# Kernel tuning notes

Measured on AMD Instinct MI355X. Metric: run time of the kernel, lower is better.

Reference implementation:

```python
import jax, jax.numpy as jnp
import numpy as np

M, K, L, OUT = 16, 64, 6, 128
IN_CH = 2 + 1 + 1 + 1 + 4 * L  # 29
HID_IN = 128 * 2 + 4           # 260


def setup_inputs() -> dict:
    key = jax.random.key(0)
    ks = jax.random.split(key, 5)
    N = 2_000_000
    P = jax.random.normal(ks[0], (N, 2), jnp.float32) * 2.0
    def lin(k, i, o):
        return jax.random.normal(k, (i, o), jnp.float32) / np.float32(np.sqrt(i))
    return {
        'P': P,
        'W1': lin(ks[1], IN_CH, 64), 'b1': jnp.zeros((64,), jnp.float32),
        'W2': lin(ks[2], 64, 128),   'b2': jnp.zeros((128,), jnp.float32),
        'W3': lin(ks[3], HID_IN, 128), 'b3': jnp.zeros((128,), jnp.float32),
        'W4': lin(ks[4], 128, OUT),  'b4': jnp.zeros((OUT,), jnp.float32),
    }


def _fps(P, m):
    # furthest point sampling, seeded at index 0 (standard convention)
    N = P.shape[0]
    def step(carry, _):
        min_d, last_idx = carry
        last = P[last_idx]
        d = jnp.sum((P - last) ** 2, axis=-1)          # [N]
        min_d = jnp.minimum(min_d, d)
        nxt = jnp.argmax(min_d)
        return (min_d, nxt), last_idx
    init = (jnp.full((N,), jnp.finfo(jnp.float32).max, jnp.float32), jnp.int32(0))
    (_, _), idxs = jax.lax.scan(step, init, None, length=m)
    return idxs  # [m] int


def _gelu(x):
    return jax.nn.gelu(x, approximate=False)  # torch nn.GELU default = erf


def reference(P, W1, b1, W2, b2, W3, b3, W4, b4):
    c_idx = jax.lax.stop_gradient(_fps(P, M))
    C = P[c_idx]                                       # [M,2]
    # brute-force kNN: expanded squared distance avoids [M,N,2] intermediate
    Ps = jax.lax.stop_gradient(P)
    Cs = jax.lax.stop_gradient(C)
    d2 = (jnp.sum(Ps ** 2, -1)[None, :]
          - 2.0 * Cs @ Ps.T
          + jnp.sum(Cs ** 2, -1)[:, None])             # [M,N]
    _, nidx = jax.lax.top_k(-d2, K)                    # [M,K]
    patch = P[nidx]                                    # [M,K,2]
    delta = patch - C[:, None, :]                      # [M,K,2]
    r = jnp.linalg.norm(delta, axis=-1, keepdims=True) # [M,K,1]
    theta = jnp.arctan2(delta[..., 1:2], delta[..., 0:1])
    freqs = (2.0 ** jnp.arange(L)).astype(jnp.float32) # [L]
    ang = delta[..., None, :] * freqs[:, None]         # [M,K,L,2]
    ff = jnp.concatenate([jnp.sin(ang), jnp.cos(ang)], -1).reshape(M, K, 4 * L)
    per_pt = jnp.concatenate([delta, r, jnp.sin(theta), jnp.cos(theta), ff], -1)  # [M,K,29]
    h = _gelu(per_pt @ W1 + b1)
    h = _gelu(h @ W2 + b2)                             # [M,K,128]
    h_max = h.max(axis=1)
    h_mean = h.mean(axis=1)
    rr = r[..., 0]                                     # [M,K]
    stats = jnp.stack([rr.mean(1), rr.max(1), rr.min(1), rr.std(1, ddof=1)], -1)  # [M,4]
    z = jnp.concatenate([h_max, h_mean, stats], -1)    # [M,260]
    F = _gelu(z @ W3 + b3) @ W4 + b4                   # [M,OUT]
    return F, C
```

## Files before the change

kernel.cpp:

```cpp
#include <hip/hip_runtime.h>
#include <math.h>

#define MCENT 16
#define KNN   64
#define NBINS 512
#define RBINS 256
#define CAP   7936
#define SKEYS 1024
#define FPSB  512
#define FPST  256
#define NPT   16
#define MLPT  1024

__device__ __forceinline__ float gelu_f(float x){
    return 0.5f * x * (1.0f + erff(x * 0.70710678118654752440f));
}

__device__ __forceinline__ void xcd_slice(int NP, int B, int bid, int tpb, int tid,
                                          int* q0, int* s1, int* step){
    int xcd = bid & 7, j = bid >> 3, Bx = B >> 3;
    long long np = NP;
    *q0   = (int)((np * xcd) >> 3) + j*tpb + tid;
    *s1   = (int)((np * (xcd+1)) >> 3);
    *step = Bx * tpb;
}

__global__ void init_kernel(unsigned int* __restrict__ ghist,
                            unsigned int* __restrict__ cnt,
                            unsigned long long* __restrict__ partials){
    const int T = gridDim.x * blockDim.x;
    int t = blockIdx.x * blockDim.x + threadIdx.x;
    for (int i = t; i < MCENT*NBINS; i += T) ghist[i] = 0u;
    for (int i = t; i < (MCENT-1)*FPSB; i += T) partials[i] = 0ULL;
    if (t < MCENT) cnt[t] = 0u;
}

__global__ __launch_bounds__(FPST, 2) void fps_coop(
    const float* __restrict__ P, int N,
    unsigned long long* __restrict__ partials,
    float* __restrict__ cxy,
    float* __restrict__ outC)
{
    const int T = FPSB * FPST;
    const int t = blockIdx.x * FPST + threadIdx.x;
    const int lane = threadIdx.x & 63;
    const int wid  = threadIdx.x >> 6;

    float px[NPT], py[NPT], md[NPT];
#pragma unroll
    for (int i = 0; i < NPT; ++i){
        int g = t + i * T;
        if (g < N){
            float2 p = ((const float2*)P)[g];
            px[i] = p.x; py[i] = p.y; md[i] = 3.402823466e+38f;
        } else { px[i] = 0.f; py[i] = 0.f; md[i] = -1.0f; }
    }

    __shared__ unsigned long long wred[FPST/64];
    int cur = 0;

    for (int k = 0; k < MCENT; ++k){
        if (blockIdx.x == 0 && threadIdx.x == 0){
            float cx = P[2*cur], cy = P[2*cur+1];
            cxy[2*k] = cx; cxy[2*k+1] = cy;
            outC[2*k] = cx; outC[2*k+1] = cy;
        }
        if (k == MCENT-1) break;

        const float cx = P[2*cur], cy = P[2*cur+1];
        unsigned long long bk = 0ULL;
#pragma unroll
        for (int i = 0; i < NPT; ++i){
            float dx = __fsub_rn(px[i], cx);
            float dy = __fsub_rn(py[i], cy);
            float d  = __fadd_rn(__fmul_rn(dx,dx), __fmul_rn(dy,dy));
            if (md[i] >= 0.0f){
                float nm = fminf(md[i], d);
                md[i] = nm;
                unsigned long long key =
                    ((unsigned long long)__float_as_uint(nm) << 32)
                    | (unsigned long long)(0xFFFFFFFFu - (unsigned)(t + i*T));
                if (key > bk) bk = key;
            }
        }
#pragma unroll
        for (int off = 32; off > 0; off >>= 1){
            unsigned long long o = __shfl_xor(bk, off, 64);
            if (o > bk) bk = o;
        }
        if (lane == 0) wred[wid] = bk;
        __syncthreads();
        if (threadIdx.x == 0){
            unsigned long long b = wred[0];
#pragma unroll
            for (int w = 1; w < FPST/64; ++w) if (wred[w] > b) b = wred[w];
            __hip_atomic_store(&partials[k*FPSB + blockIdx.x], b,
                               __ATOMIC_RELEASE, __HIP_MEMORY_SCOPE_AGENT);
        }
        __syncthreads();

        unsigned long long pb = 0ULL;
        for (int i = threadIdx.x; i < FPSB; i += FPST){
            const unsigned long long* slot = &partials[k*FPSB + i];
            unsigned long long v = __hip_atomic_load(slot, __ATOMIC_RELAXED,
                                                     __HIP_MEMORY_SCOPE_AGENT);
            while (v == 0ULL){
                __builtin_amdgcn_s_sleep(1);
                v = __hip_atomic_load(slot, __ATOMIC_RELAXED,
                                      __HIP_MEMORY_SCOPE_AGENT);
            }
            if (v > pb) pb = v;
        }
#pragma unroll
        for (int off = 32; off > 0; off >>= 1){
            unsigned long long o = __shfl_xor(pb, off, 64);
            if (o > pb) pb = o;
        }
        if (lane == 0) wred[wid] = pb;
        __syncthreads();
        unsigned long long fin = wred[0];
#pragma unroll
        for (int w = 1; w < FPST/64; ++w) if (wred[w] > fin) fin = wred[w];
        __syncthreads();
        cur = (int)(0xFFFFFFFFu - (unsigned)(fin & 0xFFFFFFFFu));
    }
}

__global__ __launch_bounds__(256) void hist_kernel(
    const float* __restrict__ P, int N,
    const float* __restrict__ cxy,
    unsigned int* __restrict__ ghist,
    unsigned int* __restrict__ rhist)
{
    __shared__ unsigned int h[MCENT*NBINS];
    __shared__ float scx[MCENT], scy[MCENT], scs2[MCENT];
    {
        int gi = blockIdx.x*blockDim.x + threadIdx.x;
        if (gi < MCENT*RBINS) rhist[gi] = 0u;
    }
    for (int i = threadIdx.x; i < MCENT*NBINS; i += blockDim.x) h[i] = 0u;
    if (threadIdx.x < MCENT){
        float a = cxy[2*threadIdx.x], b = cxy[2*threadIdx.x+1];
        scx[threadIdx.x] = a; scy[threadIdx.x] = b;
        scs2[threadIdx.x] = __fadd_rn(__fmul_rn(a,a), __fmul_rn(b,b));
    }
    __syncthreads();
    const int T    = gridDim.x * blockDim.x;
    const int NP16 = (N >> 1) >> 4;
    for (int q = blockIdx.x*blockDim.x + threadIdx.x; q < NP16; q += T){
        float4 p = ((const float4*)P)[(size_t)q << 4];
        float ps20 = __fadd_rn(__fmul_rn(p.x,p.x), __fmul_rn(p.y,p.y));
        float ps21 = __fadd_rn(__fmul_rn(p.z,p.z), __fmul_rn(p.w,p.w));
#pragma unroll
        for (int m = 0; m < MCENT; ++m){
            float dot0 = __fadd_rn(__fmul_rn(scx[m],p.x), __fmul_rn(scy[m],p.y));
            float d20  = __fadd_rn(__fsub_rn(ps20, __fmul_rn(2.0f,dot0)), scs2[m]);
            atomicAdd(&h[m*NBINS + (__float_as_uint(fmaxf(d20,0.0f)) >> 22)], 1u);
            float dot1 = __fadd_rn(__fmul_rn(scx[m],p.z), __fmul_rn(scy[m],p.w));
            float d21  = __fadd_rn(__fsub_rn(ps21, __fmul_rn(2.0f,dot1)), scs2[m]);
            atomicAdd(&h[m*NBINS + (__float_as_uint(fmaxf(d21,0.0f)) >> 22)], 1u);
        }
    }
    __syncthreads();
    for (int i = threadIdx.x; i < MCENT*NBINS; i += blockDim.x){
        unsigned v = h[i];
        if (v) atomicAdd(&ghist[i], v);
    }
}

__global__ void thr_kernel(const unsigned int* __restrict__ ghist,
                           float* __restrict__ sc2){
    int m = threadIdx.x;
    if (m < MCENT){
        unsigned cum = 0; int B = NBINS-1;
        for (int b = 0; b < NBINS; ++b){
            cum += ghist[m*NBINS + b];
            if (cum >= KNN){ B = b; break; }
        }
        sc2[m] = 255.0f / __uint_as_float((unsigned)(B+1) << 22);
    }
}

__global__ __launch_bounds__(256) void refine_kernel(
    const float* __restrict__ P, int N,
    const float* __restrict__ cxy,
    const float* __restrict__ sc2,
    unsigned int* __restrict__ rhist)
{
    __shared__ unsigned int h[MCENT*RBINS];
    __shared__ float scx[MCENT], scy[MCENT], scs2[MCENT], ssc[MCENT];
    for (int i = threadIdx.x; i < MCENT*RBINS; i += 256) h[i] = 0u;
    if (threadIdx.x < MCENT){
        float a = cxy[2*threadIdx.x], b = cxy[2*threadIdx.x+1];
        scx[threadIdx.x]=a; scy[threadIdx.x]=b;
        scs2[threadIdx.x]=__fadd_rn(__fmul_rn(a,a),__fmul_rn(b,b));
        ssc[threadIdx.x]=sc2[threadIdx.x];
    }
    __syncthreads();
    const int NP = N >> 1;
    int q0, s1, st;
    xcd_slice(NP, gridDim.x, blockIdx.x, 256, threadIdx.x, &q0, &s1, &st);
    for (int q = q0; q < s1; q += st){
        float4 p = ((const float4*)P)[q];
        float ps20 = __fadd_rn(__fmul_rn(p.x,p.x), __fmul_rn(p.y,p.y));
        float ps21 = __fadd_rn(__fmul_rn(p.z,p.z), __fmul_rn(p.w,p.w));
#pragma unroll
        for (int m = 0; m < MCENT; ++m){
            float dot0 = __fadd_rn(__fmul_rn(scx[m],p.x), __fmul_rn(scy[m],p.y));
            float d20  = __fadd_rn(__fsub_rn(ps20, __fmul_rn(2.0f,dot0)), scs2[m]);
            int b0 = (int)(fmaxf(d20, 0.0f) * ssc[m]);
            if (b0 < RBINS) atomicAdd(&h[m*RBINS + b0], 1u);
            float dot1 = __fadd_rn(__fmul_rn(scx[m],p.z), __fmul_rn(scy[m],p.w));
            float d21  = __fadd_rn(__fsub_rn(ps21, __fmul_rn(2.0f,dot1)), scs2[m]);
            int b1 = (int)(fmaxf(d21, 0.0f) * ssc[m]);
            if (b1 < RBINS) atomicAdd(&h[m*RBINS + b1], 1u);
        }
    }
    if ((N & 1) && blockIdx.x == 0 && threadIdx.x == 0){
        int g = N-1;
        float x = P[2*g], y = P[2*g+1];
        float ps2 = __fadd_rn(__fmul_rn(x,x), __fmul_rn(y,y));
        for (int m = 0; m < MCENT; ++m){
            float dot = __fadd_rn(__fmul_rn(scx[m],x), __fmul_rn(scy[m],y));
            float d2  = __fadd_rn(__fsub_rn(ps2, __fmul_rn(2.0f,dot)), scs2[m]);
            int b = (int)(fmaxf(d2, 0.0f) * ssc[m]);
            if (b < RBINS) atomicAdd(&h[m*RBINS + b], 1u);
        }
    }
    __syncthreads();
    for (int i = threadIdx.x; i < MCENT*RBINS; i += blockDim.x){
        unsigned v = h[i];
        if (v) atomicAdd(&rhist[i], v);
    }
}

__global__ void thr2_kernel(const unsigned int* __restrict__ rhist,
                            int* __restrict__ B2){
    int m = threadIdx.x;
    if (m < MCENT){
        unsigned cum = 0; int B = RBINS-1;
        for (int b = 0; b < RBINS; ++b){
            cum += rhist[m*RBINS + b];
            if (cum >= KNN){ B = b; break; }
        }
        B2[m] = B;
    }
}

__global__ __launch_bounds__(256) void collect_kernel(
    const float* __restrict__ P, int N,
    const float* __restrict__ cxy,
    const float* __restrict__ sc2,
    const int* __restrict__ B2,
    unsigned int* __restrict__ cnt,
    float* __restrict__ cd2,
    int* __restrict__ cidx)
{
    __shared__ float scx[MCENT], scy[MCENT], scs2[MCENT], ssc[MCENT];
    __shared__ int sB2[MCENT];
    if (threadIdx.x < MCENT){
        float a = cxy[2*threadIdx.x], b = cxy[2*threadIdx.x+1];
        scx[threadIdx.x]=a; scy[threadIdx.x]=b;
        scs2[threadIdx.x]=__fadd_rn(__fmul_rn(a,a),__fmul_rn(b,b));
        ssc[threadIdx.x]=sc2[threadIdx.x];
        sB2[threadIdx.x]=B2[threadIdx.x];
    }
    __syncthreads();
    const int NP = N >> 1;
    int q0, s1, st;
    xcd_slice(NP, gridDim.x, blockIdx.x, 256, threadIdx.x, &q0, &s1, &st);
    for (int q = q0; q < s1; q += st){
        float4 p = ((const float4*)P)[q];
        float ps20 = __fadd_rn(__fmul_rn(p.x,p.x), __fmul_rn(p.y,p.y));
        float ps21 = __fadd_rn(__fmul_rn(p.z,p.z), __fmul_rn(p.w,p.w));
        int g = 2*q;
#pragma unroll
        for (int m = 0; m < MCENT; ++m){
            float dot0 = __fadd_rn(__fmul_rn(scx[m],p.x), __fmul_rn(scy[m],p.y));
            float d20  = __fadd_rn(__fsub_rn(ps20, __fmul_rn(2.0f,dot0)), scs2[m]);
            if ((int)(fmaxf(d20,0.0f) * ssc[m]) <= sB2[m]){
                unsigned pos = atomicAdd(&cnt[m], 1u);
                if (pos < CAP){ cd2[m*CAP+pos]=d20; cidx[m*CAP+pos]=g; }
            }
            float dot1 = __fadd_rn(__fmul_rn(scx[m],p.z), __fmul_rn(scy[m],p.w));
            float d21  = __fadd_rn(__fsub_rn(ps21, __fmul_rn(2.0f,dot1)), scs2[m]);
            if ((int)(fmaxf(d21,0.0f) * ssc[m]) <= sB2[m]){
                unsigned pos = atomicAdd(&cnt[m], 1u);
                if (pos < CAP){ cd2[m*CAP+pos]=d21; cidx[m*CAP+pos]=g+1; }
            }
        }
    }
    if ((N & 1) && blockIdx.x == 0 && threadIdx.x == 0){
        int g = N-1;
        float x = P[2*g], y = P[2*g+1];
        float ps2 = __fadd_rn(__fmul_rn(x,x), __fmul_rn(y,y));
        for (int m = 0; m < MCENT; ++m){
            float dot = __fadd_rn(__fmul_rn(scx[m],x), __fmul_rn(scy[m],y));
            float d2  = __fadd_rn(__fsub_rn(ps2, __fmul_rn(2.0f,dot)), scs2[m]);
            if ((int)(fmaxf(d2,0.0f) * ssc[m]) <= sB2[m]){
                unsigned pos = atomicAdd(&cnt[m], 1u);
                if (pos < CAP){ cd2[m*CAP+pos]=d2; cidx[m*CAP+pos]=g; }
            }
        }
    }
}

__global__ __launch_bounds__(MLPT) void mlp_kernel(
    const float* __restrict__ P,
    const float* __restrict__ cxy,
    const unsigned int* __restrict__ cnt,
    const float* __restrict__ cd2,
    const int* __restrict__ cidx,
    const float* __restrict__ W1, const float* __restrict__ b1,
    const float* __restrict__ W2, const float* __restrict__ b2,
    const float* __restrict__ W3, const float* __restrict__ b3,
    const float* __restrict__ W4, const float* __restrict__ b4,
    float* __restrict__ outF)
{
    const int m = blockIdx.x;
    const int tid = threadIdx.x;
    __shared__ float feat[KNN][32];
    __shared__ float h1s[KNN][64];
    __shared__ float sW1[29*64];
    __shared__ float sW2[64*128];
    __shared__ float pmax[8][128], psum[8][128];
    __shared__ float z[260];
    __shared__ float part[8][128];
    __shared__ float zz[128];
    __shared__ unsigned long long kkeys[SKEYS];
    __shared__ int snbr[KNN];

    {
        const float4* s2 = (const float4*)W2;
        float4* d2 = (float4*)sW2;
        d2[tid]        = s2[tid];
        d2[tid + 1024] = s2[tid + 1024];
        if (tid < 464) ((float4*)sW1)[tid] = ((const float4*)W1)[tid];
    }

    unsigned c = cnt[m]; if (c > CAP) c = CAP;
    if (c <= SKEYS){
        if (tid < (int)c){
            unsigned u = __float_as_uint(cd2[m*CAP+tid]);
            u = (u & 0x80000000u) ? ~u : (u | 0x80000000u);
            kkeys[tid] = ((unsigned long long)u << 32)
                       | (unsigned long long)(unsigned)cidx[m*CAP+tid];
        }
        __syncthreads();
        if (tid < (int)c){
            unsigned long long ki = kkeys[tid];
            int rank = 0;
            for (int j = 0; j < (int)c; ++j) rank += (kkeys[j] < ki);
            if (rank < KNN) snbr[rank] = (int)(unsigned)(ki & 0xFFFFFFFFu);
        }
    } else {
        for (int i = tid; i < (int)c; i += MLPT){
            unsigned ui = __float_as_uint(cd2[m*CAP+i]);
            ui = (ui & 0x80000000u) ? ~ui : (ui | 0x80000000u);
            unsigned long long ki = ((unsigned long long)ui << 32)
                                  | (unsigned long long)(unsigned)cidx[m*CAP+i];
            int rank = 0;
            for (int j = 0; j < (int)c; ++j){
                unsigned uj = __float_as_uint(cd2[m*CAP+j]);
                uj = (uj & 0x80000000u) ? ~uj : (uj | 0x80000000u);
                unsigned long long kj = ((unsigned long long)uj << 32)
                                      | (unsigned long long)(unsigned)cidx[m*CAP+j];
                rank += (kj < ki);
            }
            if (rank < KNN) snbr[rank] = (int)(unsigned)(ki & 0xFFFFFFFFu);
        }
    }
    __syncthreads();

    const float cx = cxy[2*m], cy = cxy[2*m+1];
    if (tid < KNN){
        int g = snbr[tid];
        float dx = P[2*g]   - cx;
        float dy = P[2*g+1] - cy;
        float r  = sqrtf(dx*dx + dy*dy);
        float th = atan2f(dy, dx);
        feat[tid][0]=dx; feat[tid][1]=dy; feat[tid][2]=r;
        feat[tid][3]=sinf(th); feat[tid][4]=cosf(th);
        float fx = dx, fy = dy;
#pragma unroll
        for (int l = 0; l < 6; ++l){
            feat[tid][5+4*l+0]=sinf(fx);
            feat[tid][5+4*l+1]=sinf(fy);
            feat[tid][5+4*l+2]=cosf(fx);
            feat[tid][5+4*l+3]=cosf(fy);
            fx += fx; fy += fy;
        }
    }
    __syncthreads();

#pragma unroll
    for (int rep = 0; rep < 4; ++rep){
        int o = rep*MLPT + tid;
        int k = o >> 6, j = o & 63;
        float acc = b1[j];
#pragma unroll
        for (int cc = 0; cc < 29; ++cc) acc += feat[k][cc] * sW1[cc*64 + j];
        h1s[k][j] = gelu_f(acc);
    }
    __syncthreads();

    {
        int j = tid & 127, kh = tid >> 7;
        float lmax = -3.402823466e+38f, lsum = 0.f;
        for (int kk = 0; kk < 8; ++kk){
            int k = kh*8 + kk;
            float acc = b2[j];
#pragma unroll 8
            for (int i = 0; i < 64; ++i) acc += h1s[k][i] * sW2[i*128 + j];
            float v = gelu_f(acc);
            lmax = fmaxf(lmax, v);
            lsum += v;
        }
        pmax[kh][j] = lmax; psum[kh][j] = lsum;
    }
    __syncthreads();
    if (tid < 128){
        float mx = pmax[0][tid], sm = psum[0][tid];
#pragma unroll
        for (int w = 1; w < 8; ++w){ mx = fmaxf(mx, pmax[w][tid]); sm += psum[w][tid]; }
        z[tid]       = mx;
        z[128 + tid] = sm * (1.0f/64.0f);
    }
    if (tid >= 128 && tid < 192){
        int l = tid - 128;
        float r = feat[l][2];
        float s = r, mx = r, mn = r;
        for (int off = 1; off < 64; off <<= 1){
            s  += __shfl_xor(s, off, 64);
            mx  = fmaxf(mx, __shfl_xor(mx, off, 64));
            mn  = fminf(mn, __shfl_xor(mn, off, 64));
        }
        float mean = s * (1.0f/64.0f);
        float dv = (r-mean)*(r-mean);
        for (int off = 1; off < 64; off <<= 1) dv += __shfl_xor(dv, off, 64);
        if (l == 0){
            z[256]=mean; z[257]=mx; z[258]=mn; z[259]=sqrtf(dv*(1.0f/63.0f));
        }
    }
    __syncthreads();

    {
        int j = tid & 127, seg = tid >> 7;
        int i0  = (seg < 4) ? seg*33 : 132 + (seg-4)*32;
        int cntn = (seg < 4) ? 33 : 32;
        float acc = 0.f;
        for (int i = i0; i < i0 + cntn; ++i) acc += z[i]*W3[i*128+j];
        part[seg][j] = acc;
    }
    __syncthreads();
    if (tid < 128){
        float a = part[0][tid];
#pragma unroll
        for (int w = 1; w < 8; ++w) a += part[w][tid];
        zz[tid] = gelu_f(a + b3[tid]);
    }
    __syncthreads();
    {
        int j = tid & 127, seg = tid >> 7;
        float acc = 0.f;
#pragma unroll
        for (int i = seg*16; i < seg*16+16; ++i) acc += zz[i]*W4[i*128+j];
        part[seg][j] = acc;
    }
    __syncthreads();
    if (tid < 128){
        float a = part[0][tid];
#pragma unroll
        for (int w = 1; w < 8; ++w) a += part[w][tid];
        outF[m*128 + tid] = a + b4[tid];
    }
}

extern "C" void kernel_launch(void* const* d_in, const int* in_sizes, int n_in,
                              void* d_out, int out_size, void* d_ws, size_t ws_size,
                              hipStream_t stream)
{
    const float* P  = (const float*)d_in[0];
    const float* W1 = (const float*)d_in[1];
    const float* b1 = (const float*)d_in[2];
    const float* W2 = (const float*)d_in[3];
    const float* b2 = (const float*)d_in[4];
    const float* W3 = (const float*)d_in[5];
    const float* b3 = (const float*)d_in[6];
    const float* W4 = (const float*)d_in[7];
    const float* b4 = (const float*)d_in[8];
    int N = in_sizes[0] / 2;
    float* outF = (float*)d_out;
    float* outC = outF + MCENT*128;
    (void)n_in; (void)out_size; (void)ws_size;

    char* base = (char*)d_ws;
    size_t off = 0;
    auto take = [&](size_t bytes)->char*{
        char* p = base + off;
        off = (off + bytes + 255) & ~(size_t)255;
        return p;
    };
    unsigned long long* partials = (unsigned long long*)take((size_t)(MCENT-1)*FPSB*8);
    float* cxy         = (float*)take(MCENT*2*4);
    unsigned int* ghist= (unsigned int*)take(MCENT*NBINS*4);
    unsigned int* rhist= (unsigned int*)take(MCENT*RBINS*4);
    unsigned int* cnt  = (unsigned int*)take(MCENT*4);
    float* sc2         = (float*)take(MCENT*4);
    int*   B2          = (int*)  take(MCENT*4);
    float* cd2         = (float*)take((size_t)MCENT*CAP*4);
    int*   cidx        = (int*)  take((size_t)MCENT*CAP*4);

    init_kernel<<<32, 256, 0, stream>>>(ghist, cnt, partials);

    void* fargs[] = { (void*)&P, (void*)&N, (void*)&partials,
                      (void*)&cxy, (void*)&outC };
    hipLaunchCooperativeKernel((const void*)fps_coop, dim3(FPSB), dim3(FPST),
                               fargs, 0, stream);

    hist_kernel<<<128, 256, 0, stream>>>(P, N, cxy, ghist, rhist);
    thr_kernel<<<1, 64, 0, stream>>>(ghist, sc2);
    refine_kernel<<<1024, 256, 0, stream>>>(P, N, cxy, sc2, rhist);
    thr2_kernel<<<1, 64, 0, stream>>>(rhist, B2);
    collect_kernel<<<1024, 256, 0, stream>>>(P, N, cxy, sc2, B2, cnt, cd2, cidx);
    mlp_kernel<<<MCENT, MLPT, 0, stream>>>(P, cxy, cnt, cd2, cidx,
                                           W1,b1,W2,b2,W3,b3,W4,b4, outF);
}
```

Before: 379.0 us.

## Reduce FPS block partials in one block and broadcast the argmax index

```diff
diff --git a/kernel.cpp b/kernel.cpp
--- a/kernel.cpp
+++ b/kernel.cpp
@@ -27,17 +27,20 @@
 
 __global__ void init_kernel(unsigned int* __restrict__ ghist,
                             unsigned int* __restrict__ cnt,
-                            unsigned long long* __restrict__ partials){
+                            unsigned long long* __restrict__ partials,
+                            unsigned int* __restrict__ bcast){
     const int T = gridDim.x * blockDim.x;
     int t = blockIdx.x * blockDim.x + threadIdx.x;
     for (int i = t; i < MCENT*NBINS; i += T) ghist[i] = 0u;
     for (int i = t; i < (MCENT-1)*FPSB; i += T) partials[i] = 0ULL;
     if (t < MCENT) cnt[t] = 0u;
+    if (t < MCENT) bcast[t] = 0u;
 }
 
 __global__ __launch_bounds__(FPST, 2) void fps_coop(
     const float* __restrict__ P, int N,
     unsigned long long* __restrict__ partials,
+    unsigned int* __restrict__ bcast,
     float* __restrict__ cxy,
     float* __restrict__ outC)
 {
@@ -57,6 +60,7 @@
     }
 
     __shared__ unsigned long long wred[FPST/64];
+    __shared__ int s_cur;
     int cur = 0;
 
     for (int k = 0; k < MCENT; ++k){
@@ -99,30 +103,50 @@
         }
         __syncthreads();
 
-        unsigned long long pb = 0ULL;
-        for (int i = threadIdx.x; i < FPSB; i += FPST){
-            const unsigned long long* slot = &partials[k*FPSB + i];
-            unsigned long long v = __hip_atomic_load(slot, __ATOMIC_RELAXED,
-                                                     __HIP_MEMORY_SCOPE_AGENT);
-            while (v == 0ULL){
-                __builtin_amdgcn_s_sleep(1);
-                v = __hip_atomic_load(slot, __ATOMIC_RELAXED,
-                                      __HIP_MEMORY_SCOPE_AGENT);
-            }
-            if (v > pb) pb = v;
-        }
-#pragma unroll
-        for (int off = 32; off > 0; off >>= 1){
-            unsigned long long o = __shfl_xor(pb, off, 64);
-            if (o > pb) pb = o;
-        }
-        if (lane == 0) wred[wid] = pb;
-        __syncthreads();
-        unsigned long long fin = wred[0];
-#pragma unroll
-        for (int w = 1; w < FPST/64; ++w) if (wred[w] > fin) fin = wred[w];
-        __syncthreads();
-        cur = (int)(0xFFFFFFFFu - (unsigned)(fin & 0xFFFFFFFFu));
+        if (blockIdx.x == 0){
+            unsigned long long pb = 0ULL;
+            for (int i = threadIdx.x; i < FPSB; i += FPST){
+                const unsigned long long* slot = &partials[k*FPSB + i];
+                unsigned long long v = __hip_atomic_load(slot, __ATOMIC_RELAXED,
+                                                         __HIP_MEMORY_SCOPE_AGENT);
+                while (v == 0ULL){
+                    __builtin_amdgcn_s_sleep(2);
+                    v = __hip_atomic_load(slot, __ATOMIC_RELAXED,
+                                          __HIP_MEMORY_SCOPE_AGENT);
+                }
+                if (v > pb) pb = v;
+            }
+#pragma unroll
+            for (int off = 32; off > 0; off >>= 1){
+                unsigned long long o = __shfl_xor(pb, off, 64);
+                if (o > pb) pb = o;
+            }
+            if (lane == 0) wred[wid] = pb;
+            __syncthreads();
+            if (threadIdx.x == 0){
+                unsigned long long fin = wred[0];
+#pragma unroll
+                for (int w = 1; w < FPST/64; ++w) if (wred[w] > fin) fin = wred[w];
+                int c = (int)(0xFFFFFFFFu - (unsigned)(fin & 0xFFFFFFFFu));
+                s_cur = c;
+                __hip_atomic_store(&bcast[k], (unsigned)(c + 1),
+                                   __ATOMIC_RELEASE, __HIP_MEMORY_SCOPE_AGENT);
+            }
+            __syncthreads();
+        } else {
+            if (threadIdx.x == 0){
+                unsigned v = __hip_atomic_load(&bcast[k], __ATOMIC_RELAXED,
+                                               __HIP_MEMORY_SCOPE_AGENT);
+                while (v == 0u){
+                    __builtin_amdgcn_s_sleep(4);
+                    v = __hip_atomic_load(&bcast[k], __ATOMIC_RELAXED,
+                                          __HIP_MEMORY_SCOPE_AGENT);
+                }
+                s_cur = (int)v - 1;
+            }
+            __syncthreads();
+        }
+        cur = s_cur;
     }
 }
 
@@ -502,6 +526,7 @@
         return p;
     };
     unsigned long long* partials = (unsigned long long*)take((size_t)(MCENT-1)*FPSB*8);
+    unsigned int* bcast = (unsigned int*)take(MCENT*4);
     float* cxy         = (float*)take(MCENT*2*4);
     unsigned int* ghist= (unsigned int*)take(MCENT*NBINS*4);
     unsigned int* rhist= (unsigned int*)take(MCENT*RBINS*4);
@@ -511,9 +536,9 @@
     float* cd2         = (float*)take((size_t)MCENT*CAP*4);
     int*   cidx        = (int*)  take((size_t)MCENT*CAP*4);
 
-    init_kernel<<<32, 256, 0, stream>>>(ghist, cnt, partials);
-
-    void* fargs[] = { (void*)&P, (void*)&N, (void*)&partials,
+    init_kernel<<<32, 256, 0, stream>>>(ghist, cnt, partials, bcast);
+
+    void* fargs[] = { (void*)&P, (void*)&N, (void*)&partials, (void*)&bcast,
                       (void*)&cxy, (void*)&outC };
     hipLaunchCooperativeKernel((const void*)fps_coop, dim3(FPSB), dim3(FPST),
                                fargs, 0, stream);
```

Result: faster. 341.2 us (-10.0%).
